# Kernel tuning notes

Hardware: AMD Instinct MI355X
Metric: run time of the kernel (lower is better)

The kernel has to match this reference:

```python
import jax, jax.numpy as jnp
import numpy as np
import math

D_MODEL = 1024
N_HEADS = 16
FFN_DIM = 4096
B, L = 8, 1024
LN_EPS = 1e-5


def setup_inputs() -> dict:
    key = jax.random.key(0)
    ks = jax.random.split(key, 16)
    s = 1.0 / math.sqrt(D_MODEL)
    sf = 1.0 / math.sqrt(FFN_DIM)
    # weights stored [in, out] (transposed vs torch nn.Linear)
    return {
        "x": jax.random.normal(ks[0], (B, L, D_MODEL), dtype=jnp.float32),
        "Wq": jax.random.normal(ks[1], (D_MODEL, D_MODEL), dtype=jnp.float32) * s,
        "bq": jnp.zeros((D_MODEL,), jnp.float32),
        "Wk": jax.random.normal(ks[2], (D_MODEL, D_MODEL), dtype=jnp.float32) * s,
        "bk": jnp.zeros((D_MODEL,), jnp.float32),
        "Wv": jax.random.normal(ks[3], (D_MODEL, D_MODEL), dtype=jnp.float32) * s,
        "bv": jnp.zeros((D_MODEL,), jnp.float32),
        "Wo": jax.random.normal(ks[4], (D_MODEL, D_MODEL), dtype=jnp.float32) * s,
        "bo": jnp.zeros((D_MODEL,), jnp.float32),
        "W1": jax.random.normal(ks[5], (D_MODEL, FFN_DIM), dtype=jnp.float32) * s,
        "b1": jnp.zeros((FFN_DIM,), jnp.float32),
        "W2": jax.random.normal(ks[6], (FFN_DIM, D_MODEL), dtype=jnp.float32) * sf,
        "b2": jnp.zeros((D_MODEL,), jnp.float32),
        "gamma": jnp.ones((D_MODEL,), jnp.float32),
        "beta": jnp.zeros((D_MODEL,), jnp.float32),
    }


def reference(x, Wq, bq, Wk, bk, Wv, bv, Wo, bo, W1, b1, W2, b2, gamma, beta):
    Bb, Ll, D = x.shape
    H = N_HEADS
    E = D // H
    scale = 1.0 / math.sqrt(E)
    # multi-head attention (dropout is identity in eval)
    q = (x @ Wq + bq).reshape(Bb, Ll, H, E)
    k = (x @ Wk + bk).reshape(Bb, Ll, H, E)
    v = (x @ Wv + bv).reshape(Bb, Ll, H, E)
    scores = jnp.einsum('blhe,bshe->bhls', q, k)  # [B,H,L,L]
    A = jax.nn.softmax(scale * scores, axis=-1)
    ctx = jnp.einsum('bhls,bshd->blhd', A, v).reshape(Bb, Ll, D)
    attn_out = ctx @ Wo + bo
    x = x + attn_out
    # FFN: conv1d kernel_size=1 == pointwise linear; exact (erf) GELU as in F.gelu
    h = jax.nn.gelu(x @ W1 + b1, approximate=False)
    x = x + (h @ W2 + b2)
    # LayerNorm
    mu = jnp.mean(x, axis=-1, keepdims=True)
    var = jnp.mean(jnp.square(x - mu), axis=-1, keepdims=True)
    out = (x - mu) * jax.lax.rsqrt(var + LN_EPS) * gamma + beta
    return out
```

## Files before the change

### kernel.cpp

```cpp
#include <hip/hip_runtime.h>
#include <cmath>

typedef __attribute__((ext_vector_type(8))) _Float16 half8;
typedef __attribute__((ext_vector_type(4))) _Float16 half4;
typedef __attribute__((ext_vector_type(4))) float f32x4;

__device__ __forceinline__ void glds16(const void* g, void* l) {
  __builtin_amdgcn_global_load_lds(
      (__attribute__((address_space(1))) const void*)g,
      (__attribute__((address_space(3))) void*)l, 16, 0, 0);
}

__device__ __forceinline__ float fast_erf(float x) {
  float ax = fabsf(x);
  float t = 1.0f / (1.0f + 0.3275911f * ax);
  float y = t * (0.254829592f +
            t * (-0.284496736f +
            t * (1.421413741f +
            t * (-1.453152027f + t * 1.061405429f))));
  float r = 1.0f - y * __expf(-ax * ax);
  return copysignf(r, x);
}

__global__ __launch_bounds__(256) void k_prep(
    const float* __restrict__ x, _Float16* __restrict__ xb,
    const float* __restrict__ Wq, const float* __restrict__ Wk,
    const float* __restrict__ Wv, const float* __restrict__ Wo,
    const float* __restrict__ W1, const float* __restrict__ W2,
    _Float16* __restrict__ Wqkvt, _Float16* __restrict__ Wot,
    _Float16* __restrict__ W1t, _Float16* __restrict__ W2t,
    const float* __restrict__ bq, const float* __restrict__ bk,
    const float* __restrict__ bv, float* __restrict__ bqkv) {
  __shared__ float t[64][65];
  const int tid = threadIdx.x;
  const int bid = blockIdx.x;
  if (bid < 4096) {
    int i = (bid * 256 + tid) * 8;
    const f32x4* p = (const f32x4*)(x + i);
    f32x4 a = p[0], b = p[1];
    half8 h;
    h[0] = (_Float16)a[0]; h[1] = (_Float16)a[1]; h[2] = (_Float16)a[2]; h[3] = (_Float16)a[3];
    h[4] = (_Float16)b[0]; h[5] = (_Float16)b[1]; h[6] = (_Float16)b[2]; h[7] = (_Float16)b[3];
    *(half8*)(xb + i) = h;
    return;
  }
  const int tt = bid - 4096;
  if (tt >= 3072) {
    int i = (tt - 3072) * 256 + tid;
    const float* s = i < 1024 ? bq : (i < 2048 ? bk : bv);
    bqkv[i] = s[i & 1023];
    return;
  }
  const float* W; _Float16* Wt; int K, N, bx, by;
  if (tt < 1024) {
    const int wsel = tt >> 8, r = tt & 255;
    W = wsel == 0 ? Wq : wsel == 1 ? Wk : wsel == 2 ? Wv : Wo;
    Wt = wsel < 3 ? Wqkvt + (size_t)wsel * 1024 * 1024 : Wot;
    K = 1024; N = 1024; bx = r & 15; by = r >> 4;
  } else if (tt < 2048) {
    const int r = tt - 1024;
    W = W1; Wt = W1t; K = 1024; N = 4096; bx = r & 63; by = r >> 6;
  } else {
    const int r = tt - 2048;
    W = W2; Wt = W2t; K = 4096; N = 1024; bx = r & 15; by = r >> 4;
  }
  const int k0 = by << 6, n0 = bx << 6;
  {
    const int r = tid >> 2, q = tid & 3;
    const float* src = &W[(size_t)(k0 + r) * N + n0 + q * 16];
    f32x4 v0 = *(const f32x4*)(src);
    f32x4 v1 = *(const f32x4*)(src + 4);
    f32x4 v2 = *(const f32x4*)(src + 8);
    f32x4 v3 = *(const f32x4*)(src + 12);
    float* d = &t[r][q * 16];
#pragma unroll
    for (int j = 0; j < 4; ++j) d[j] = v0[j];
#pragma unroll
    for (int j = 0; j < 4; ++j) d[4 + j] = v1[j];
#pragma unroll
    for (int j = 0; j < 4; ++j) d[8 + j] = v2[j];
#pragma unroll
    for (int j = 0; j < 4; ++j) d[12 + j] = v3[j];
  }
  __syncthreads();
#pragma unroll
  for (int p = 0; p < 2; ++p) {
    const int c = p * 256 + tid;
    const int row = c >> 3, c8 = c & 7;
    half8 hv;
#pragma unroll
    for (int j = 0; j < 8; ++j) hv[j] = (_Float16)t[c8 * 8 + j][row];
    *(half8*)&Wt[(size_t)(n0 + row) * K + k0 + c8 * 8] = hv;
  }
}

template <int BM, int EPI>
__global__ __launch_bounds__(512, 2) void k_gemm8(
    const _Float16* __restrict__ A, const _Float16* __restrict__ Bt,
    const float* __restrict__ bias, const float* __restrict__ res,
    float* __restrict__ outf, _Float16* __restrict__ outh, int M, int N, int K) {
  constexpr int MR = BM / 32;
  constexpr int MH2 = MR / 2;
  constexpr int AL = BM * 64;
  constexpr int BL = 256 * 64;
  constexpr int ABYTES = BM * 128;
  constexpr int BBYTES = 256 * 128;
  constexpr int AB2 = 2 * ABYTES;
  __shared__ _Float16 lds[2 * (AL + BL)];
  const char* ldsc = (const char*)lds;

  const int tid = threadIdx.x;
  const int lane = tid & 63;
  const int w = tid >> 6, wr = w >> 2, wc = w & 3;
  const int l15 = lane & 15, grp = lane >> 4;

  const int gx = gridDim.x;
  const int nwg = gx * gridDim.y;
  const int lid = blockIdx.y * gx + blockIdx.x;
  const int wid = (lid & 7) * (nwg >> 3) + (lid >> 3);
  const int m0 = (wid / gx) * BM, n0 = (wid % gx) * 256;

  const int m2 = (l15 >> 2) & 1, m01 = l15 & 3;
  const int chunk0 = (m2 << 2) | (grp ^ m01);
  const int aoff0 = wr * 2048 + l15 * 128 + chunk0 * 16;
  const int aoff1 = aoff0 ^ 64;
  const int boff0 = wc * 2048 + l15 * 128 + chunk0 * 16;
  const int boff1 = boff0 ^ 64;

  const int srow = tid >> 3;
  const int scs8 = ((tid & 7) ^ (srow & 7)) * 8;
  const int NK = K >> 6;

  f32x4 acc[MR][4] = {};
  half8 af[MH2][2], bf[2][2];

#define STG_A(J, MHH, KN)                                                      \
  _Pragma("unroll") for (int s = 0; s < BM / 128; ++s)                         \
      glds16(A + (size_t)(m0 + (MHH) * (BM / 2) + s * 64 + srow) * K +         \
                 (size_t)(KN)*64 + scs8,                                       \
             lds + (J)*AL + ((MHH) * (BM / 2) + s * 64) * 64 + tid * 8);
#define STG_B(J, NHH, KN)                                                      \
  _Pragma("unroll") for (int s = 0; s < 2; ++s)                                \
      glds16(Bt + (size_t)(n0 + (NHH)*128 + s * 64 + srow) * K +               \
                  (size_t)(KN)*64 + scs8,                                      \
             lds + 2 * AL + (J)*BL + ((NHH)*128 + s * 64) * 64 + tid * 8);

#define VM_8 asm volatile("s_waitcnt vmcnt(8)" ::: "memory")
#define VM_6 asm volatile("s_waitcnt vmcnt(6)" ::: "memory")
#define VM_NONE

#define PHASE(J, MHQ, NHQ, RA, RB, STGSTMT, VMSTMT)                            \
  {                                                                            \
    if constexpr (RA) {                                                        \
      _Pragma("unroll") for (int i = 0; i < MH2; ++i) {                        \
        af[i][0] = *(const half8*)(ldsc + (J)*ABYTES +                         \
                                   ((MHQ)*MH2 + i) * 4096 + aoff0);            \
        af[i][1] = *(const half8*)(ldsc + (J)*ABYTES +                         \
                                   ((MHQ)*MH2 + i) * 4096 + aoff1);            \
      }                                                                        \
    }                                                                          \
    if constexpr (RB) {                                                        \
      _Pragma("unroll") for (int n = 0; n < 2; ++n) {                          \
        bf[n][0] = *(const half8*)(ldsc + AB2 + (J)*BBYTES +                   \
                                   ((NHQ)*2 + n) * 8192 + boff0);              \
        bf[n][1] = *(const half8*)(ldsc + AB2 + (J)*BBYTES +                   \
                                   ((NHQ)*2 + n) * 8192 + boff1);              \
      }                                                                        \
    }                                                                          \
    STGSTMT;                                                                   \
    __builtin_amdgcn_s_barrier();                                              \
    asm volatile("s_waitcnt lgkmcnt(0)");                                      \
    __builtin_amdgcn_sched_barrier(0);                                         \
    __builtin_amdgcn_s_setprio(1);                                             \
    _Pragma("unroll") for (int ks = 0; ks < 2; ++ks)                           \
        _Pragma("unroll") for (int i = 0; i < MH2; ++i)                        \
            _Pragma("unroll") for (int n = 0; n < 2; ++n)                      \
                acc[(MHQ)*MH2 + i][(NHQ)*2 + n] =                              \
                    __builtin_amdgcn_mfma_f32_16x16x32_f16(                    \
                        af[i][ks], bf[n][ks], acc[(MHQ)*MH2 + i][(NHQ)*2 + n], \
                        0, 0, 0);                                              \
    __builtin_amdgcn_s_setprio(0);                                             \
    VMSTMT;                                                                    \
    __builtin_amdgcn_s_barrier();                                              \
  }

#define KTILE(J, KT)                                                           \
  {                                                                            \
    const int kn1_ = ((KT) + 1 < NK) ? (KT) + 1 : NK - 1;                      \
    const int kn2_ = ((KT) + 2 < NK) ? (KT) + 2 : NK - 1;                      \
    PHASE(J, 0, 0, true, true, STG_B(1 - (J), 0, kn1_), VM_NONE)               \
    PHASE(J, 0, 1, false, true, STG_A(1 - (J), 1, kn1_), VM_8)                 \
    PHASE(J, 1, 1, true, false, STG_A(J, 0, kn2_), VM_NONE)                    \
    PHASE(J, 1, 0, false, true, STG_B(J, 1, kn2_), VM_6)                       \
  }

  STG_A(0, 0, 0) STG_B(0, 0, 0) STG_B(0, 1, 0) STG_A(0, 1, 0)
  STG_A(1, 0, 1) STG_B(1, 1, 1)
  VM_6;
  __builtin_amdgcn_s_barrier();

#pragma unroll 1
  for (int kt = 0; kt < NK; kt += 2) {
    KTILE(0, kt)
    KTILE(1, kt + 1)
  }
  asm volatile("s_waitcnt vmcnt(0)" ::: "memory");
#undef KTILE
#undef PHASE
#undef VM_8
#undef VM_6
#undef VM_NONE
#undef STG_A
#undef STG_B

  float bcol[4];
#pragma unroll
  for (int n = 0; n < 4; ++n) bcol[n] = bias[n0 + (n * 4 + wc) * 16 + l15];
#pragma unroll
  for (int m = 0; m < MR; ++m) {
#pragma unroll
    for (int rr = 0; rr < 4; ++rr) {
      const size_t row = m0 + (m * 2 + wr) * 16 + grp * 4 + rr;
#pragma unroll
      for (int n = 0; n < 4; ++n) {
        const int col = n0 + (n * 4 + wc) * 16 + l15;
        float v = acc[m][n][rr] + bcol[n];
        const size_t idx = row * N + col;
        if (EPI == 0) {
          outh[idx] = (_Float16)v;
        } else if (EPI == 1) {
          float t2 = v + res[idx];
          outf[idx] = t2;
          outh[idx] = (_Float16)t2;
        } else if (EPI == 2) {
          float g = 0.5f * v * (1.0f + fast_erf(v * 0.70710678118654752f));
          outh[idx] = (_Float16)g;
        } else {
          outf[idx] = v + res[idx];
        }
      }
    }
  }
}

template <int EPI>
__global__ __launch_bounds__(512, 2) void k_gemmf(
    const _Float16* __restrict__ A, const _Float16* __restrict__ Bt,
    const float* __restrict__ bias, const void* __restrict__ res,
    float* __restrict__ outf, _Float16* __restrict__ outh, int M, int N, int K) {
  constexpr int AL = 256 * 64, BL = 128 * 64;
  constexpr int ABY = 32768, BBY = 16384, BBASE = 3 * ABY;
  __shared__ _Float16 lds[3 * (AL + BL)];
  const char* ldsc = (const char*)lds;

  const int tid = threadIdx.x;
  const int lane = tid & 63;
  const int w = tid >> 6, wr = w >> 1, wc = w & 1;
  const int l15 = lane & 15, grp = lane >> 4;

  const int gx = gridDim.x;
  const int nwg = gx * gridDim.y;
  const int lid = blockIdx.y * gx + blockIdx.x;
  const int wid = (lid & 7) * (nwg >> 3) + (lid >> 3);
  const int m0 = (wid / gx) * 256, n0 = (wid % gx) * 128;

  const int m2 = (l15 >> 2) & 1, m01 = l15 & 3;
  const int c0 = ((m2 << 2) | (grp ^ m01)) * 16;
  const int aoff0 = wr * 2048 + l15 * 128 + c0;
  const int aoff1 = aoff0 ^ 64;
  const int boff0 = wc * 2048 + l15 * 128 + c0;
  const int boff1 = boff0 ^ 64;

  const int srow = tid >> 3;
  const int scs8 = ((tid & 7) ^ (srow & 7)) * 8;
  const int NK = K >> 6;

  const _Float16* aG = A + (size_t)(m0 + srow) * K + scs8;
  const _Float16* bG = Bt + (size_t)(n0 + srow) * K + scs8;

  f32x4 acc[4][4] = {};

#define FSTG_A(JJ, HH, KN)                                                     \
  _Pragma("unroll") for (int s = 0; s < 2; ++s)                                \
      glds16(aG + (size_t)((HH)*128 + s * 64) * K + (size_t)(KN)*64,           \
             lds + (JJ)*AL + ((HH)*128 + s * 64) * 64 + tid * 8);
#define FSTG_B(JJ, HH, KN)                                                     \
  glds16(bG + (size_t)((HH)*64) * K + (size_t)(KN)*64,                         \
         lds + 3 * AL + (JJ)*BL + (HH)*64 * 64 + tid * 8);

#define FPHASE(PA, PB, AO, BO, STGSTMT, VMSTMT)                                \
  {                                                                            \
    half8 af_[4], bf_[4];                                                      \
    _Pragma("unroll") for (int m = 0; m < 4; ++m)                              \
        af_[m] = *(const half8*)((PA) + m * 8192 + (AO));                      \
    _Pragma("unroll") for (int n = 0; n < 4; ++n)                              \
        bf_[n] = *(const half8*)((PB) + n * 4096 + (BO));                      \
    STGSTMT;                                                                   \
    __builtin_amdgcn_s_barrier();                                              \
    asm volatile("s_waitcnt lgkmcnt(0)");                                      \
    __builtin_amdgcn_sched_barrier(0);                                         \
    __builtin_amdgcn_s_setprio(1);                                             \
    _Pragma("unroll") for (int m = 0; m < 4; ++m)                              \
        _Pragma("unroll") for (int n = 0; n < 4; ++n)                          \
            acc[m][n] = __builtin_amdgcn_mfma_f32_16x16x32_f16(                \
                af_[m], bf_[n], acc[m][n], 0, 0, 0);                           \
    __builtin_amdgcn_s_setprio(0);                                             \
    VMSTMT;                                                                    \
    __builtin_amdgcn_s_barrier();                                              \
  }

  FSTG_A(0, 0, 0) FSTG_A(0, 1, 0) FSTG_B(0, 0, 0) FSTG_B(0, 1, 0)
  FSTG_A(1, 0, 1) FSTG_A(1, 1, 1) FSTG_B(1, 0, 1) FSTG_B(1, 1, 1)
  asm volatile("s_waitcnt vmcnt(6)" ::: "memory");
  __builtin_amdgcn_s_barrier();

  int j = 0, j2 = 2;
#pragma unroll 1
  for (int kt = 0; kt < NK; ++kt) {
    const int kn = (kt + 2 < NK) ? kt + 2 : NK - 1;
    const char* pa = ldsc + j * ABY;
    const char* pb = ldsc + BBASE + j * BBY;
    FPHASE(pa, pb, aoff0, boff0, { FSTG_A(j2, 0, kn) FSTG_B(j2, 0, kn) }, )
    FPHASE(pa, pb, aoff1, boff1, { FSTG_A(j2, 1, kn) FSTG_B(j2, 1, kn) },
           asm volatile("s_waitcnt vmcnt(6)" ::: "memory");)
    j = (j == 2) ? 0 : j + 1;
    j2 = (j2 == 2) ? 0 : j2 + 1;
  }
  asm volatile("s_waitcnt vmcnt(0)" ::: "memory");
#undef FPHASE
#undef FSTG_A
#undef FSTG_B

  float bcol[4];
#pragma unroll
  for (int n = 0; n < 4; ++n) bcol[n] = bias[n0 + (n * 2 + wc) * 16 + l15];
  if (EPI == 5) {
    const float QSC = 0.125f * 1.44269504088896f;
    _Float16* vt = (_Float16*)outf;
#pragma unroll
    for (int m = 0; m < 4; ++m) {
#pragma unroll
      for (int n = 0; n < 4; ++n) {
        const int col = n0 + (n * 2 + wc) * 16 + l15;
        const size_t row0 = m0 + (m * 4 + wr) * 16 + grp * 4;
        if (col < 2048) {
          const float scl = (col < 1024) ? QSC : 1.0f;
#pragma unroll
          for (int rr = 0; rr < 4; ++rr)
            outh[(row0 + rr) * (size_t)N + col] = (_Float16)((acc[m][n][rr] + bcol[n]) * scl);
        } else {
          const int b = (int)(row0 >> 10), s = (int)(row0 & 1023);
          const int cv = col - 2048, hh = cv >> 6, e = cv & 63;
          half4 pk;
#pragma unroll
          for (int rr = 0; rr < 4; ++rr) pk[rr] = (_Float16)(acc[m][n][rr] + bcol[n]);
          *(half4*)&vt[((size_t)((b << 4) | hh) * 64 + e) * 1024 + s] = pk;
        }
      }
    }
    return;
  }
#pragma unroll
  for (int m = 0; m < 4; ++m) {
#pragma unroll
    for (int rr = 0; rr < 4; ++rr) {
      const size_t row = m0 + (m * 4 + wr) * 16 + grp * 4 + rr;
#pragma unroll
      for (int n = 0; n < 4; ++n) {
        const int col = n0 + (n * 2 + wc) * 16 + l15;
        float v = acc[m][n][rr] + bcol[n];
        const size_t idx = row * N + col;
        if (EPI == 0) {
          outh[idx] = (_Float16)v;
        } else if (EPI == 1) {
          float t2 = v + ((const float*)res)[idx];
          outh[idx] = (_Float16)t2;
        } else if (EPI == 2) {
          float g = 0.5f * v * (1.0f + fast_erf(v * 0.70710678118654752f));
          outh[idx] = (_Float16)g;
        } else {
          float t2 = v + (float)((const _Float16*)res)[idx];
          outf[idx] = t2;
        }
      }
    }
  }
}

__global__ __launch_bounds__(256) void k_attn(const _Float16* __restrict__ qkv,
                                              const _Float16* __restrict__ Vt,
                                              _Float16* __restrict__ ctx) {
  __shared__ _Float16 Ks[128 * 64];
  __shared__ _Float16 Vs[64 * 128];
  __shared__ _Float16 Ps[4][16 * 136];
  const int tid = threadIdx.x;
  const int lane = tid & 63, w = tid >> 6;
  const int l15 = lane & 15, grp = lane >> 4;
  const int d = blockIdx.x;
  const int bh = (d & 7) * 16 + ((d >> 3) & 15);
  const int q0 = (d >> 7) << 7;
  const int b = bh >> 4, h = bh & 15;

  half8 qf[2][2];
#pragma unroll
  for (int qs = 0; qs < 2; ++qs) {
    const _Float16* qp =
        qkv + (size_t)(b * 1024 + q0 + qs * 64 + w * 16 + l15) * 3072 + h * 64 + grp * 8;
    qf[qs][0] = *(const half8*)qp;
    qf[qs][1] = *(const half8*)(qp + 32);
  }
  half8 ones;
#pragma unroll
  for (int i = 0; i < 8; ++i) ones[i] = (_Float16)1.0f;

  f32x4 octx[2][4] = {};
  f32x4 lsum[2] = {};
  float mrun[2] = {-1e30f, -1e30f};

  for (int kt = 0; kt < 8; ++kt) {
    const int s0 = kt * 128;
#pragma unroll
    for (int i = 0; i < 4; ++i) {
      {
        int srow = i * 32 + (tid >> 3);
        int c8 = (tid & 7) ^ (srow & 7);
        glds16(qkv + (size_t)(b * 1024 + s0 + srow) * 3072 + 1024 + h * 64 + c8 * 8,
               Ks + w * 512 + i * 2048);
      }
      {
        int erow = i * 16 + (tid >> 4);
        int c16 = (tid & 15) ^ (erow & 7);
        glds16(Vt + (size_t)(bh * 64 + erow) * 1024 + s0 + c16 * 8,
               Vs + w * 512 + i * 2048);
      }
    }
    __syncthreads();
#pragma unroll
    for (int qs = 0; qs < 2; ++qs) {
      f32x4 sacc[8] = {};
      __builtin_amdgcn_s_setprio(1);
#pragma unroll
      for (int ks = 0; ks < 2; ++ks)
#pragma unroll
        for (int f = 0; f < 8; ++f) {
          int srow = f * 16 + l15;
          half8 kf = *(const half8*)&Ks[srow * 64 + ((ks * 32 + grp * 8) ^ ((srow & 7) * 8))];
          sacc[f] = __builtin_amdgcn_mfma_f32_16x16x32_f16(kf, qf[qs][ks], sacc[f], 0, 0, 0);
        }
      __builtin_amdgcn_s_setprio(0);
      float tmax = -1e30f;
#pragma unroll
      for (int f = 0; f < 8; ++f)
#pragma unroll
        for (int r = 0; r < 4; ++r) tmax = fmaxf(tmax, sacc[f][r]);
      tmax = fmaxf(tmax, __shfl_xor(tmax, 16));
      tmax = fmaxf(tmax, __shfl_xor(tmax, 32));
      if (!__all(tmax <= mrun[qs] + 8.0f)) {
        float mnew = fmaxf(mrun[qs], tmax);
        float corr = exp2f(mrun[qs] - mnew);
        mrun[qs] = mnew;
#pragma unroll
        for (int r = 0; r < 4; ++r) {
          float cq = __shfl(corr, (lane & 48) + grp * 4 + r);
#pragma unroll
          for (int jf = 0; jf < 4; ++jf) octx[qs][jf][r] *= cq;
          lsum[qs][r] *= cq;
        }
      }
#pragma unroll
      for (int f = 0; f < 8; ++f) {
        half4 pk;
#pragma unroll
        for (int r = 0; r < 4; ++r) pk[r] = (_Float16)exp2f(sacc[f][r] - mrun[qs]);
        *(half4*)&Ps[w][l15 * 136 + f * 16 + grp * 4] = pk;
      }
      __builtin_amdgcn_s_setprio(1);
#pragma unroll
      for (int ks2 = 0; ks2 < 4; ++ks2) {
        half8 pa = *(const half8*)&Ps[w][l15 * 136 + ks2 * 32 + grp * 8];
        lsum[qs] = __builtin_amdgcn_mfma_f32_16x16x32_f16(pa, ones, lsum[qs], 0, 0, 0);
#pragma unroll
        for (int jf = 0; jf < 4; ++jf) {
          int erow = jf * 16 + l15;
          half8 vb = *(const half8*)&Vs[erow * 128 + ((ks2 * 32 + grp * 8) ^ ((erow & 7) * 8))];
          octx[qs][jf] = __builtin_amdgcn_mfma_f32_16x16x32_f16(pa, vb, octx[qs][jf], 0, 0, 0);
        }
      }
      __builtin_amdgcn_s_setprio(0);
    }
    __syncthreads();
  }
#pragma unroll
  for (int qs = 0; qs < 2; ++qs) {
#pragma unroll
    for (int r = 0; r < 4; ++r) {
      float inv = 1.0f / lsum[qs][r];
      const size_t row = b * 1024 + q0 + qs * 64 + w * 16 + grp * 4 + r;
#pragma unroll
      for (int jf = 0; jf < 4; ++jf)
        ctx[row * 1024 + h * 64 + jf * 16 + l15] = (_Float16)(octx[qs][jf][r] * inv);
    }
  }
}

__global__ __launch_bounds__(256) void k_ln(const float* xin, const float* __restrict__ gamma,
                                            const float* __restrict__ beta, float* out) {
  __shared__ float red[8];
  const int tid = threadIdx.x;
  const size_t row = blockIdx.x;
  f32x4 v = *(const f32x4*)&xin[row * 1024 + tid * 4];
  float s = v[0] + v[1] + v[2] + v[3];
  float s2 = v[0] * v[0] + v[1] * v[1] + v[2] * v[2] + v[3] * v[3];
#pragma unroll
  for (int o = 32; o >= 1; o >>= 1) {
    s += __shfl_xor(s, o);
    s2 += __shfl_xor(s2, o);
  }
  if ((tid & 63) == 0) { red[tid >> 6] = s; red[4 + (tid >> 6)] = s2; }
  __syncthreads();
  s = red[0] + red[1] + red[2] + red[3];
  s2 = red[4] + red[5] + red[6] + red[7];
  float mu = s * (1.0f / 1024.0f);
  float var = s2 * (1.0f / 1024.0f) - mu * mu;
  float rs = rsqrtf(var + 1e-5f);
  f32x4 g = *(const f32x4*)&gamma[tid * 4];
  f32x4 bt = *(const f32x4*)&beta[tid * 4];
  f32x4 o4;
#pragma unroll
  for (int r = 0; r < 4; ++r) o4[r] = (v[r] - mu) * rs * g[r] + bt[r];
  *(f32x4*)&out[row * 1024 + tid * 4] = o4;
}

extern "C" void kernel_launch(void* const* d_in, const int* in_sizes, int n_in,
                              void* d_out, int out_size, void* d_ws, size_t ws_size,
                              hipStream_t stream) {
  (void)in_sizes; (void)n_in; (void)out_size; (void)ws_size;
  const float* x  = (const float*)d_in[0];
  const float* Wq = (const float*)d_in[1];  const float* bq = (const float*)d_in[2];
  const float* Wk = (const float*)d_in[3];  const float* bk = (const float*)d_in[4];
  const float* Wv = (const float*)d_in[5];  const float* bv = (const float*)d_in[6];
  const float* Wo = (const float*)d_in[7];  const float* bo = (const float*)d_in[8];
  const float* W1 = (const float*)d_in[9];  const float* b1 = (const float*)d_in[10];
  const float* W2 = (const float*)d_in[11]; const float* b2 = (const float*)d_in[12];
  const float* gamma = (const float*)d_in[13];
  const float* beta  = (const float*)d_in[14];
  float* out = (float*)d_out;

  char* p = (char*)d_ws;
  _Float16* xb    = (_Float16*)p;  p += (size_t)16 << 20;
  _Float16* qkv   = (_Float16*)p;
  _Float16* hbuf  = (_Float16*)p;  p += (size_t)48 << 20;
  _Float16* Vt    = (_Float16*)p;  p += (size_t)16 << 20;
  _Float16* Wqkvt = (_Float16*)p;  p += (size_t)3072 * 1024 * 2;
  _Float16* Wot   = (_Float16*)p;  p += (size_t)1024 * 1024 * 2;
  _Float16* W1t   = (_Float16*)p;  p += (size_t)4096 * 1024 * 2;
  _Float16* W2t   = (_Float16*)p;  p += (size_t)4096 * 1024 * 2;
  float*    bqkv  = (float*)p;     p += (size_t)3072 * 4;
  _Float16* x1b   = (_Float16*)p;  p += (size_t)16 << 20;
  _Float16* ctx   = xb;

  k_prep<<<7180, 256, 0, stream>>>(x, xb, Wq, Wk, Wv, Wo, W1, W2,
                                   Wqkvt, Wot, W1t, W2t, bq, bk, bv, bqkv);

  k_gemmf<5><<<dim3(24, 32), 512, 0, stream>>>(xb, Wqkvt, bqkv, nullptr, (float*)Vt, qkv,
                                               8192, 3072, 1024);
  k_attn<<<1024, 256, 0, stream>>>(qkv, Vt, ctx);
  k_gemmf<1><<<dim3(8, 32), 512, 0, stream>>>(ctx, Wot, bo, x, nullptr, x1b,
                                              8192, 1024, 1024);
  k_gemm8<256, 2><<<dim3(16, 32), 512, 0, stream>>>(x1b, W1t, b1, nullptr, nullptr, hbuf,
                                                    8192, 4096, 1024);
  k_gemmf<4><<<dim3(8, 32), 512, 0, stream>>>(hbuf, W2t, b2, x1b, out, nullptr,
                                              8192, 1024, 4096);
  k_ln<<<8192, 256, 0, stream>>>(out, gamma, beta, out);
}
```

Before: 331.8 us.

## Double-buffer attention K/V tiles and read fp16 residual in Wo epilogue

The attention kernel now uses 64-key tiles in two LDS buffers. The next tile is prefetched with async global-to-LDS loads while the current one is computed, using explicit vmcnt waits and raw barriers in place of __syncthreads. Separately, ctx gets its own workspace buffer so the fp16 copy of x (xb) survives, and the Wo GEMM epilogue reads that half-precision residual instead of the fp32 x, halving residual read bytes. The residual add in fp16 adds some rounding error, and the extra ctx buffer uses more workspace.

```diff
diff --git a/kernel.cpp b/kernel.cpp
--- a/kernel.cpp
+++ b/kernel.cpp
@@ -373,7 +373,7 @@
         if (EPI == 0) {
           outh[idx] = (_Float16)v;
         } else if (EPI == 1) {
-          float t2 = v + ((const float*)res)[idx];
+          float t2 = v + (float)((const _Float16*)res)[idx];
           outh[idx] = (_Float16)t2;
         } else if (EPI == 2) {
           float g = 0.5f * v * (1.0f + fast_erf(v * 0.70710678118654752f));
@@ -390,9 +390,9 @@
 __global__ __launch_bounds__(256) void k_attn(const _Float16* __restrict__ qkv,
                                               const _Float16* __restrict__ Vt,
                                               _Float16* __restrict__ ctx) {
-  __shared__ _Float16 Ks[128 * 64];
-  __shared__ _Float16 Vs[64 * 128];
-  __shared__ _Float16 Ps[4][16 * 136];
+  __shared__ _Float16 Ks[2][64 * 64];
+  __shared__ _Float16 Vs[2][64 * 64];
+  __shared__ _Float16 Ps[4][16 * 68];
   const int tid = threadIdx.x;
   const int lane = tid & 63, w = tid >> 6;
   const int l15 = lane & 15, grp = lane >> 4;
@@ -417,40 +417,43 @@
   f32x4 lsum[2] = {};
   float mrun[2] = {-1e30f, -1e30f};
 
-  for (int kt = 0; kt < 8; ++kt) {
-    const int s0 = kt * 128;
-#pragma unroll
-    for (int i = 0; i < 4; ++i) {
-      {
-        int srow = i * 32 + (tid >> 3);
-        int c8 = (tid & 7) ^ (srow & 7);
-        glds16(qkv + (size_t)(b * 1024 + s0 + srow) * 3072 + 1024 + h * 64 + c8 * 8,
-               Ks + w * 512 + i * 2048);
-      }
-      {
-        int erow = i * 16 + (tid >> 4);
-        int c16 = (tid & 15) ^ (erow & 7);
-        glds16(Vt + (size_t)(bh * 64 + erow) * 1024 + s0 + c16 * 8,
-               Vs + w * 512 + i * 2048);
-      }
+#define ASTAGE(BB, S0)                                                         \
+  _Pragma("unroll") for (int i = 0; i < 2; ++i) {                              \
+    int sr = i * 32 + (tid >> 3);                                              \
+    int c8 = (tid & 7) ^ (sr & 7);                                             \
+    glds16(qkv + (size_t)(b * 1024 + (S0) + sr) * 3072 + 1024 + h * 64 + c8 * 8, \
+           &Ks[BB][0] + i * 2048 + tid * 8);                                   \
+    glds16(Vt + (size_t)(bh * 64 + sr) * 1024 + (S0) + c8 * 8,                 \
+           &Vs[BB][0] + i * 2048 + tid * 8);                                   \
+  }
+
+  ASTAGE(0, 0)
+#pragma unroll 1
+  for (int kt = 0; kt < 16; ++kt) {
+    const int bb = kt & 1;
+    if (kt + 1 < 16) {
+      ASTAGE(1 - bb, (kt + 1) * 64)
+      asm volatile("s_waitcnt vmcnt(4)" ::: "memory");
+    } else {
+      asm volatile("s_waitcnt vmcnt(0)" ::: "memory");
     }
-    __syncthreads();
+    __builtin_amdgcn_s_barrier();
 #pragma unroll
     for (int qs = 0; qs < 2; ++qs) {
-      f32x4 sacc[8] = {};
+      f32x4 sacc[4] = {};
       __builtin_amdgcn_s_setprio(1);
 #pragma unroll
       for (int ks = 0; ks < 2; ++ks)
 #pragma unroll
-        for (int f = 0; f < 8; ++f) {
-          int srow = f * 16 + l15;
-          half8 kf = *(const half8*)&Ks[srow * 64 + ((ks * 32 + grp * 8) ^ ((srow & 7) * 8))];
+        for (int f = 0; f < 4; ++f) {
+          int sr = f * 16 + l15;
+          half8 kf = *(const half8*)&Ks[bb][sr * 64 + ((ks * 32 + grp * 8) ^ ((sr & 7) * 8))];
           sacc[f] = __builtin_amdgcn_mfma_f32_16x16x32_f16(kf, qf[qs][ks], sacc[f], 0, 0, 0);
         }
       __builtin_amdgcn_s_setprio(0);
       float tmax = -1e30f;
 #pragma unroll
-      for (int f = 0; f < 8; ++f)
+      for (int f = 0; f < 4; ++f)
 #pragma unroll
         for (int r = 0; r < 4; ++r) tmax = fmaxf(tmax, sacc[f][r]);
       tmax = fmaxf(tmax, __shfl_xor(tmax, 16));
@@ -468,28 +471,29 @@
         }
       }
 #pragma unroll
-      for (int f = 0; f < 8; ++f) {
+      for (int f = 0; f < 4; ++f) {
         half4 pk;
 #pragma unroll
         for (int r = 0; r < 4; ++r) pk[r] = (_Float16)exp2f(sacc[f][r] - mrun[qs]);
-        *(half4*)&Ps[w][l15 * 136 + f * 16 + grp * 4] = pk;
+        *(half4*)&Ps[w][l15 * 68 + f * 16 + grp * 4] = pk;
       }
       __builtin_amdgcn_s_setprio(1);
 #pragma unroll
-      for (int ks2 = 0; ks2 < 4; ++ks2) {
-        half8 pa = *(const half8*)&Ps[w][l15 * 136 + ks2 * 32 + grp * 8];
+      for (int ks2 = 0; ks2 < 2; ++ks2) {
+        half8 pa = *(const half8*)&Ps[w][l15 * 68 + ks2 * 32 + grp * 8];
         lsum[qs] = __builtin_amdgcn_mfma_f32_16x16x32_f16(pa, ones, lsum[qs], 0, 0, 0);
 #pragma unroll
         for (int jf = 0; jf < 4; ++jf) {
-          int erow = jf * 16 + l15;
-          half8 vb = *(const half8*)&Vs[erow * 128 + ((ks2 * 32 + grp * 8) ^ ((erow & 7) * 8))];
+          int er = jf * 16 + l15;
+          half8 vb = *(const half8*)&Vs[bb][er * 64 + ((ks2 * 32 + grp * 8) ^ ((er & 7) * 8))];
           octx[qs][jf] = __builtin_amdgcn_mfma_f32_16x16x32_f16(pa, vb, octx[qs][jf], 0, 0, 0);
         }
       }
       __builtin_amdgcn_s_setprio(0);
     }
-    __syncthreads();
-  }
+    __builtin_amdgcn_s_barrier();
+  }
+#undef ASTAGE
 #pragma unroll
   for (int qs = 0; qs < 2; ++qs) {
 #pragma unroll
@@ -551,13 +555,13 @@
   _Float16* qkv   = (_Float16*)p;
   _Float16* hbuf  = (_Float16*)p;  p += (size_t)48 << 20;
   _Float16* Vt    = (_Float16*)p;  p += (size_t)16 << 20;
+  _Float16* ctx   = (_Float16*)p;  p += (size_t)16 << 20;
   _Float16* Wqkvt = (_Float16*)p;  p += (size_t)3072 * 1024 * 2;
   _Float16* Wot   = (_Float16*)p;  p += (size_t)1024 * 1024 * 2;
   _Float16* W1t   = (_Float16*)p;  p += (size_t)4096 * 1024 * 2;
   _Float16* W2t   = (_Float16*)p;  p += (size_t)4096 * 1024 * 2;
   float*    bqkv  = (float*)p;     p += (size_t)3072 * 4;
   _Float16* x1b   = (_Float16*)p;  p += (size_t)16 << 20;
-  _Float16* ctx   = xb;
 
   k_prep<<<7180, 256, 0, stream>>>(x, xb, Wq, Wk, Wv, Wo, W1, W2,
                                    Wqkvt, Wot, W1t, W2t, bq, bk, bv, bqkv);
@@ -565,7 +569,7 @@
   k_gemmf<5><<<dim3(24, 32), 512, 0, stream>>>(xb, Wqkvt, bqkv, nullptr, (float*)Vt, qkv,
                                                8192, 3072, 1024);
   k_attn<<<1024, 256, 0, stream>>>(qkv, Vt, ctx);
-  k_gemmf<1><<<dim3(8, 32), 512, 0, stream>>>(ctx, Wot, bo, x, nullptr, x1b,
+  k_gemmf<1><<<dim3(8, 32), 512, 0, stream>>>(ctx, Wot, bo, xb, nullptr, x1b,
                                               8192, 1024, 1024);
   k_gemm8<256, 2><<<dim3(16, 32), 512, 0, stream>>>(x1b, W1t, b1, nullptr, nullptr, hbuf,
                                                     8192, 4096, 1024);
```

Result: slower. 343.5 us (+3.5%).
